# Performance work log

Hardware: AMD Instinct MI355X
Metric: run time of the kernel (lower is better)

## Reference

```python
import jax, jax.numpy as jnp
import numpy as np

DIM = 2048
SEQ = 8192
KSZ = 3  # L_cache


def setup_inputs() -> dict:
    key = jax.random.key(0)
    ks = jax.random.split(key, 6)
    s = 1.0 / np.sqrt(DIM)
    return {
        "x": jax.random.normal(ks[0], (1, SEQ, DIM), dtype=jnp.float32),
        "B_w": jax.random.normal(ks[1], (DIM, DIM), dtype=jnp.float32) * s,
        "C_w": jax.random.normal(ks[2], (DIM, DIM), dtype=jnp.float32) * s,
        "x_w": jax.random.normal(ks[3], (DIM, DIM), dtype=jnp.float32) * s,
        "out_w": jax.random.normal(ks[4], (DIM, DIM), dtype=jnp.float32) * s,
        "conv_w": jax.random.normal(ks[5], (DIM, 1, KSZ), dtype=jnp.float32) * (1.0 / np.sqrt(KSZ)),
        "conv_state": jnp.zeros((1, DIM, KSZ - 1), dtype=jnp.float32),
    }


def reference(x, B_w, C_w, x_w, out_w, conv_w, conv_state):
    # x: [1, S, D]; Linear(y = x @ W.T), then transpose to [1, D, S]
    B = jnp.einsum('bsd,ed->bes', x, B_w)   # [1, D, S]
    C = jnp.einsum('bsd,ed->bes', x, C_w)   # [1, D, S]
    xp = jnp.einsum('bsd,ed->bes', x, x_w)  # [1, D, S]

    Bx = B * xp                                          # gated input [1, D, S]
    Bxp = jnp.concatenate([conv_state, Bx], axis=-1)     # [1, D, S + K - 1]

    # depthwise causal conv1d, kernel size K, groups = D
    conv_out = jax.lax.conv_general_dilated(
        Bxp, conv_w,
        window_strides=(1,), padding='VALID',
        dimension_numbers=('NCH', 'OIH', 'NCH'),
        feature_group_count=DIM,
    )  # [1, D, S]

    y = C * conv_out                              # output gate [1, D, S]
    y = jnp.swapaxes(y, -1, -2)                   # [1, S, D]
    return jnp.einsum('bsd,ed->bse', y, out_w)    # out_proj [1, S, D]
```

## Files before the change

### kernel.cpp

```cpp
#include <hip/hip_runtime.h>
#include <hip/hip_bf16.h>
#include <cstdint>
#include <cstddef>

#define D_DIM 2048
#define S_SEQ 8192

typedef __attribute__((ext_vector_type(8))) short bf16x8;
typedef __attribute__((ext_vector_type(4))) float f32x4;

__device__ inline unsigned short f2b(float f) {
    __hip_bfloat16 h = __float2bfloat16(f);
    return __builtin_bit_cast(unsigned short, h);
}
__device__ inline float b2f(unsigned short u) {
    return __bfloat162float(__builtin_bit_cast(__hip_bfloat16, u));
}

__global__ __launch_bounds__(256)
void cast_f32_to_bf16(const float* __restrict__ in, unsigned short* __restrict__ out, int n4) {
    int stride = gridDim.x * blockDim.x;
    for (int i = blockIdx.x * blockDim.x + threadIdx.x; i < n4; i += stride) {
        float4 v = reinterpret_cast<const float4*>(in)[i];
        ushort4 o;
        o.x = f2b(v.x); o.y = f2b(v.y); o.z = f2b(v.z); o.w = f2b(v.w);
        reinterpret_cast<ushort4*>(out)[i] = o;
    }
}

template<int MODE>
__global__ __launch_bounds__(256, 2)
void gemm_bt(const unsigned short* __restrict__ A,
             const unsigned short* __restrict__ W,
             void* out,
             const unsigned short* prev,
             int M, int N, int K)
{
    __shared__ unsigned short As[128][40];
    __shared__ unsigned short Ws[128][40];

    const int t    = threadIdx.x;
    const int lane = t & 63;
    const int wave = t >> 6;
    const int wr   = wave >> 1;
    const int wc   = wave & 1;

    const int row0 = blockIdx.x * 128;
    const int col0 = blockIdx.y * 128;

    f32x4 acc[4][4] = {};

    const int rl = lane & 15;
    const int kg = (lane >> 4) * 8;

    for (int k0 = 0; k0 < K; k0 += 32) {
        #pragma unroll
        for (int r = 0; r < 2; ++r) {
            int idx = r * 256 + t;
            int row = idx >> 2;
            int col = (idx & 3) << 3;
            *reinterpret_cast<bf16x8*>(&As[row][col]) =
                *reinterpret_cast<const bf16x8*>(&A[(size_t)(row0 + row) * K + k0 + col]);
            *reinterpret_cast<bf16x8*>(&Ws[row][col]) =
                *reinterpret_cast<const bf16x8*>(&W[(size_t)(col0 + row) * K + k0 + col]);
        }
        __syncthreads();

        bf16x8 a[4], b[4];
        #pragma unroll
        for (int m = 0; m < 4; ++m)
            a[m] = *reinterpret_cast<const bf16x8*>(&As[wr * 64 + m * 16 + rl][kg]);
        #pragma unroll
        for (int n = 0; n < 4; ++n)
            b[n] = *reinterpret_cast<const bf16x8*>(&Ws[wc * 64 + n * 16 + rl][kg]);

        #pragma unroll
        for (int m = 0; m < 4; ++m)
            #pragma unroll
            for (int n = 0; n < 4; ++n)
                acc[m][n] = __builtin_amdgcn_mfma_f32_16x16x32_bf16(a[m], b[n], acc[m][n], 0, 0, 0);

        __syncthreads();
    }

    const int cr = (lane >> 4) * 4;
    const int cc = lane & 15;
    #pragma unroll
    for (int m = 0; m < 4; ++m) {
        #pragma unroll
        for (int n = 0; n < 4; ++n) {
            int gr = row0 + wr * 64 + m * 16 + cr;
            int gc = col0 + wc * 64 + n * 16 + cc;
            #pragma unroll
            for (int r = 0; r < 4; ++r) {
                size_t off = (size_t)(gr + r) * N + gc;
                float v = acc[m][n][r];
                if (MODE == 0) {
                    ((unsigned short*)out)[off] = f2b(v);
                } else if (MODE == 1) {
                    ((unsigned short*)out)[off] = f2b(v * b2f(prev[off]));
                } else {
                    ((float*)out)[off] = v;
                }
            }
        }
    }
}

__global__ __launch_bounds__(256)
void conv_gate(const unsigned short* __restrict__ bx,
               const unsigned short* __restrict__ cb,
               const float* __restrict__ conv_w,
               const float* __restrict__ state,
               unsigned short* __restrict__ y)
{
    int s  = blockIdx.x;
    int d0 = threadIdx.x << 3;

    bf16x8 vc = *reinterpret_cast<const bf16x8*>(&bx[(size_t)s * D_DIM + d0]);
    bf16x8 vC = *reinterpret_cast<const bf16x8*>(&cb[(size_t)s * D_DIM + d0]);

    float x1[8], x2[8];
    if (s >= 2) {
        bf16x8 v1 = *reinterpret_cast<const bf16x8*>(&bx[(size_t)(s - 1) * D_DIM + d0]);
        bf16x8 v2 = *reinterpret_cast<const bf16x8*>(&bx[(size_t)(s - 2) * D_DIM + d0]);
        #pragma unroll
        for (int j = 0; j < 8; ++j) { x1[j] = b2f((unsigned short)v1[j]); x2[j] = b2f((unsigned short)v2[j]); }
    } else if (s == 1) {
        bf16x8 v1 = *reinterpret_cast<const bf16x8*>(&bx[(size_t)0 * D_DIM + d0]);
        #pragma unroll
        for (int j = 0; j < 8; ++j) { x1[j] = b2f((unsigned short)v1[j]); x2[j] = state[(d0 + j) * 2 + 1]; }
    } else {
        #pragma unroll
        for (int j = 0; j < 8; ++j) { x1[j] = state[(d0 + j) * 2 + 1]; x2[j] = state[(d0 + j) * 2 + 0]; }
    }

    bf16x8 o;
    #pragma unroll
    for (int j = 0; j < 8; ++j) {
        int d = d0 + j;
        float cur = b2f((unsigned short)vc[j]);
        float co  = conv_w[d * 3 + 0] * x2[j]
                  + conv_w[d * 3 + 1] * x1[j]
                  + conv_w[d * 3 + 2] * cur;
        o[j] = (short)f2b(b2f((unsigned short)vC[j]) * co);
    }
    *reinterpret_cast<bf16x8*>(&y[(size_t)s * D_DIM + d0]) = o;
}

extern "C" void kernel_launch(void* const* d_in, const int* in_sizes, int n_in,
                              void* d_out, int out_size, void* d_ws, size_t ws_size,
                              hipStream_t stream) {
    const float* x         = (const float*)d_in[0];
    const float* B_w       = (const float*)d_in[1];
    const float* C_w       = (const float*)d_in[2];
    const float* x_w       = (const float*)d_in[3];
    const float* out_w     = (const float*)d_in[4];
    const float* conv_w    = (const float*)d_in[5];
    const float* conv_state= (const float*)d_in[6];

    const size_t SD = (size_t)S_SEQ * D_DIM;
    const size_t DD = (size_t)D_DIM * D_DIM;

    unsigned short* ws   = (unsigned short*)d_ws;
    unsigned short* xb   = ws;
    unsigned short* bwb  = xb + SD;
    unsigned short* cwb  = bwb + DD;
    unsigned short* xwb  = cwb + DD;
    unsigned short* owb  = xwb + DD;
    unsigned short* bx   = owb + DD;
    unsigned short* cbuf = bx + SD;
    unsigned short* yb   = xb;

    cast_f32_to_bf16<<<2048, 256, 0, stream>>>(x,     xb,  (int)(SD / 4));
    cast_f32_to_bf16<<<1024, 256, 0, stream>>>(B_w,   bwb, (int)(DD / 4));
    cast_f32_to_bf16<<<1024, 256, 0, stream>>>(C_w,   cwb, (int)(DD / 4));
    cast_f32_to_bf16<<<1024, 256, 0, stream>>>(x_w,   xwb, (int)(DD / 4));
    cast_f32_to_bf16<<<1024, 256, 0, stream>>>(out_w, owb, (int)(DD / 4));

    dim3 grid(S_SEQ / 128, D_DIM / 128);
    gemm_bt<0><<<grid, 256, 0, stream>>>(xb, bwb, bx,   nullptr, S_SEQ, D_DIM, D_DIM);
    gemm_bt<1><<<grid, 256, 0, stream>>>(xb, xwb, bx,   bx,      S_SEQ, D_DIM, D_DIM);
    gemm_bt<0><<<grid, 256, 0, stream>>>(xb, cwb, cbuf, nullptr, S_SEQ, D_DIM, D_DIM);

    conv_gate<<<S_SEQ, 256, 0, stream>>>(bx, cbuf, conv_w, conv_state, yb);

    gemm_bt<2><<<grid, 256, 0, stream>>>(yb, owb, d_out, nullptr, S_SEQ, D_DIM, D_DIM);
}
```

Before: 553.2 us.

## Use direct global-to-LDS loads in GEMM and move B*xp gating into conv kernel

The GEMM tile loads now use global_load_lds to write straight into unpadded LDS tiles instead of staging through registers, and the occupancy hint in launch bounds is dropped. The B*xp product is no longer fused into the second GEMM epilogue; xp is written to the output buffer as scratch, and the conv kernel computes the gate itself. The conv kernel now processes 8 sequence steps per block, carrying the previous two inputs in registers and loading conv weights once. Removing the padding may cause LDS bank conflicts on the MFMA operand reads, and the conv kernel now reads an extra tensor.

```diff
diff --git a/kernel.cpp b/kernel.cpp
--- a/kernel.cpp
+++ b/kernel.cpp
@@ -9,12 +9,19 @@
 typedef __attribute__((ext_vector_type(8))) short bf16x8;
 typedef __attribute__((ext_vector_type(4))) float f32x4;
 
+#define GAS __attribute__((address_space(1)))
+#define LAS __attribute__((address_space(3)))
+
 __device__ inline unsigned short f2b(float f) {
     __hip_bfloat16 h = __float2bfloat16(f);
     return __builtin_bit_cast(unsigned short, h);
 }
 __device__ inline float b2f(unsigned short u) {
     return __bfloat162float(__builtin_bit_cast(__hip_bfloat16, u));
+}
+
+__device__ inline void gload_lds16(const unsigned short* g, unsigned short* l) {
+    __builtin_amdgcn_global_load_lds((const GAS void*)g, (LAS void*)l, 16, 0, 0);
 }
 
 __global__ __launch_bounds__(256)
@@ -29,15 +36,14 @@
 }
 
 template<int MODE>
-__global__ __launch_bounds__(256, 2)
+__global__ __launch_bounds__(256)
 void gemm_bt(const unsigned short* __restrict__ A,
              const unsigned short* __restrict__ W,
-             void* out,
-             const unsigned short* prev,
+             void* __restrict__ out,
              int M, int N, int K)
 {
-    __shared__ unsigned short As[128][40];
-    __shared__ unsigned short Ws[128][40];
+    __shared__ unsigned short As[128 * 32];
+    __shared__ unsigned short Ws[128 * 32];
 
     const int t    = threadIdx.x;
     const int lane = t & 63;
@@ -48,6 +54,9 @@
     const int row0 = blockIdx.x * 128;
     const int col0 = blockIdx.y * 128;
 
+    const int srow = lane >> 2;
+    const int scol = (lane & 3) << 3;
+
     f32x4 acc[4][4] = {};
 
     const int rl = lane & 15;
@@ -55,24 +64,22 @@
 
     for (int k0 = 0; k0 < K; k0 += 32) {
         #pragma unroll
-        for (int r = 0; r < 2; ++r) {
-            int idx = r * 256 + t;
-            int row = idx >> 2;
-            int col = (idx & 3) << 3;
-            *reinterpret_cast<bf16x8*>(&As[row][col]) =
-                *reinterpret_cast<const bf16x8*>(&A[(size_t)(row0 + row) * K + k0 + col]);
-            *reinterpret_cast<bf16x8*>(&Ws[row][col]) =
-                *reinterpret_cast<const bf16x8*>(&W[(size_t)(col0 + row) * K + k0 + col]);
+        for (int j = 0; j < 2; ++j) {
+            const int rbase = wave * 32 + j * 16;
+            gload_lds16(&A[(size_t)(row0 + rbase + srow) * K + k0 + scol],
+                        &As[rbase * 32]);
+            gload_lds16(&W[(size_t)(col0 + rbase + srow) * K + k0 + scol],
+                        &Ws[rbase * 32]);
         }
         __syncthreads();
 
         bf16x8 a[4], b[4];
         #pragma unroll
         for (int m = 0; m < 4; ++m)
-            a[m] = *reinterpret_cast<const bf16x8*>(&As[wr * 64 + m * 16 + rl][kg]);
+            a[m] = *reinterpret_cast<const bf16x8*>(&As[(wr * 64 + m * 16 + rl) * 32 + kg]);
         #pragma unroll
         for (int n = 0; n < 4; ++n)
-            b[n] = *reinterpret_cast<const bf16x8*>(&Ws[wc * 64 + n * 16 + rl][kg]);
+            b[n] = *reinterpret_cast<const bf16x8*>(&Ws[(wc * 64 + n * 16 + rl) * 32 + kg]);
 
         #pragma unroll
         for (int m = 0; m < 4; ++m)
@@ -97,8 +104,6 @@
                 float v = acc[m][n][r];
                 if (MODE == 0) {
                     ((unsigned short*)out)[off] = f2b(v);
-                } else if (MODE == 1) {
-                    ((unsigned short*)out)[off] = f2b(v * b2f(prev[off]));
                 } else {
                     ((float*)out)[off] = v;
                 }
@@ -107,57 +112,73 @@
     }
 }
 
+#define CONV_CHUNK 8
 __global__ __launch_bounds__(256)
-void conv_gate(const unsigned short* __restrict__ bx,
-               const unsigned short* __restrict__ cb,
+void conv_gate(const unsigned short* __restrict__ Bp,
+               const unsigned short* __restrict__ XPp,
+               const unsigned short* __restrict__ Cp,
                const float* __restrict__ conv_w,
                const float* __restrict__ state,
                unsigned short* __restrict__ y)
 {
-    int s  = blockIdx.x;
-    int d0 = threadIdx.x << 3;
-
-    bf16x8 vc = *reinterpret_cast<const bf16x8*>(&bx[(size_t)s * D_DIM + d0]);
-    bf16x8 vC = *reinterpret_cast<const bf16x8*>(&cb[(size_t)s * D_DIM + d0]);
-
-    float x1[8], x2[8];
-    if (s >= 2) {
-        bf16x8 v1 = *reinterpret_cast<const bf16x8*>(&bx[(size_t)(s - 1) * D_DIM + d0]);
-        bf16x8 v2 = *reinterpret_cast<const bf16x8*>(&bx[(size_t)(s - 2) * D_DIM + d0]);
-        #pragma unroll
-        for (int j = 0; j < 8; ++j) { x1[j] = b2f((unsigned short)v1[j]); x2[j] = b2f((unsigned short)v2[j]); }
-    } else if (s == 1) {
-        bf16x8 v1 = *reinterpret_cast<const bf16x8*>(&bx[(size_t)0 * D_DIM + d0]);
-        #pragma unroll
-        for (int j = 0; j < 8; ++j) { x1[j] = b2f((unsigned short)v1[j]); x2[j] = state[(d0 + j) * 2 + 1]; }
-    } else {
-        #pragma unroll
-        for (int j = 0; j < 8; ++j) { x1[j] = state[(d0 + j) * 2 + 1]; x2[j] = state[(d0 + j) * 2 + 0]; }
-    }
-
-    bf16x8 o;
+    const int s0 = blockIdx.x * CONV_CHUNK;
+    const int d0 = threadIdx.x << 3;
+
+    float w0[8], w1[8], w2[8];
     #pragma unroll
     for (int j = 0; j < 8; ++j) {
         int d = d0 + j;
-        float cur = b2f((unsigned short)vc[j]);
-        float co  = conv_w[d * 3 + 0] * x2[j]
-                  + conv_w[d * 3 + 1] * x1[j]
-                  + conv_w[d * 3 + 2] * cur;
-        o[j] = (short)f2b(b2f((unsigned short)vC[j]) * co);
-    }
-    *reinterpret_cast<bf16x8*>(&y[(size_t)s * D_DIM + d0]) = o;
+        w0[j] = conv_w[d * 3 + 0];
+        w1[j] = conv_w[d * 3 + 1];
+        w2[j] = conv_w[d * 3 + 2];
+    }
+
+    float p1[8], p2[8];
+    if (s0 >= 2) {
+        bf16x8 b2v  = *reinterpret_cast<const bf16x8*>(&Bp [(size_t)(s0 - 2) * D_DIM + d0]);
+        bf16x8 x2v  = *reinterpret_cast<const bf16x8*>(&XPp[(size_t)(s0 - 2) * D_DIM + d0]);
+        bf16x8 b1v  = *reinterpret_cast<const bf16x8*>(&Bp [(size_t)(s0 - 1) * D_DIM + d0]);
+        bf16x8 x1v  = *reinterpret_cast<const bf16x8*>(&XPp[(size_t)(s0 - 1) * D_DIM + d0]);
+        #pragma unroll
+        for (int j = 0; j < 8; ++j) {
+            p2[j] = b2f((unsigned short)b2v[j]) * b2f((unsigned short)x2v[j]);
+            p1[j] = b2f((unsigned short)b1v[j]) * b2f((unsigned short)x1v[j]);
+        }
+    } else {
+        #pragma unroll
+        for (int j = 0; j < 8; ++j) {
+            p2[j] = state[(d0 + j) * 2 + 0];
+            p1[j] = state[(d0 + j) * 2 + 1];
+        }
+    }
+
+    for (int s = s0; s < s0 + CONV_CHUNK; ++s) {
+        bf16x8 bv = *reinterpret_cast<const bf16x8*>(&Bp [(size_t)s * D_DIM + d0]);
+        bf16x8 xv = *reinterpret_cast<const bf16x8*>(&XPp[(size_t)s * D_DIM + d0]);
+        bf16x8 cv = *reinterpret_cast<const bf16x8*>(&Cp [(size_t)s * D_DIM + d0]);
+        bf16x8 o;
+        #pragma unroll
+        for (int j = 0; j < 8; ++j) {
+            float cur = b2f((unsigned short)bv[j]) * b2f((unsigned short)xv[j]);
+            float co  = w0[j] * p2[j] + w1[j] * p1[j] + w2[j] * cur;
+            o[j] = (short)f2b(b2f((unsigned short)cv[j]) * co);
+            p2[j] = p1[j];
+            p1[j] = cur;
+        }
+        *reinterpret_cast<bf16x8*>(&y[(size_t)s * D_DIM + d0]) = o;
+    }
 }
 
 extern "C" void kernel_launch(void* const* d_in, const int* in_sizes, int n_in,
                               void* d_out, int out_size, void* d_ws, size_t ws_size,
                               hipStream_t stream) {
-    const float* x         = (const float*)d_in[0];
-    const float* B_w       = (const float*)d_in[1];
-    const float* C_w       = (const float*)d_in[2];
-    const float* x_w       = (const float*)d_in[3];
-    const float* out_w     = (const float*)d_in[4];
-    const float* conv_w    = (const float*)d_in[5];
-    const float* conv_state= (const float*)d_in[6];
+    const float* x          = (const float*)d_in[0];
+    const float* B_w        = (const float*)d_in[1];
+    const float* C_w        = (const float*)d_in[2];
+    const float* x_w        = (const float*)d_in[3];
+    const float* out_w      = (const float*)d_in[4];
+    const float* conv_w     = (const float*)d_in[5];
+    const float* conv_state = (const float*)d_in[6];
 
     const size_t SD = (size_t)S_SEQ * D_DIM;
     const size_t DD = (size_t)D_DIM * D_DIM;
@@ -170,6 +191,7 @@
     unsigned short* owb  = xwb + DD;
     unsigned short* bx   = owb + DD;
     unsigned short* cbuf = bx + SD;
+    unsigned short* xpb  = (unsigned short*)d_out;
     unsigned short* yb   = xb;
 
     cast_f32_to_bf16<<<2048, 256, 0, stream>>>(x,     xb,  (int)(SD / 4));
@@ -179,11 +201,11 @@
     cast_f32_to_bf16<<<1024, 256, 0, stream>>>(out_w, owb, (int)(DD / 4));
 
     dim3 grid(S_SEQ / 128, D_DIM / 128);
-    gemm_bt<0><<<grid, 256, 0, stream>>>(xb, bwb, bx,   nullptr, S_SEQ, D_DIM, D_DIM);
-    gemm_bt<1><<<grid, 256, 0, stream>>>(xb, xwb, bx,   bx,      S_SEQ, D_DIM, D_DIM);
-    gemm_bt<0><<<grid, 256, 0, stream>>>(xb, cwb, cbuf, nullptr, S_SEQ, D_DIM, D_DIM);
-
-    conv_gate<<<S_SEQ, 256, 0, stream>>>(bx, cbuf, conv_w, conv_state, yb);
-
-    gemm_bt<2><<<grid, 256, 0, stream>>>(yb, owb, d_out, nullptr, S_SEQ, D_DIM, D_DIM);
-}
+    gemm_bt<0><<<grid, 256, 0, stream>>>(xb, bwb, bx,   S_SEQ, D_DIM, D_DIM);
+    gemm_bt<0><<<grid, 256, 0, stream>>>(xb, xwb, xpb,  S_SEQ, D_DIM, D_DIM);
+    gemm_bt<0><<<grid, 256, 0, stream>>>(xb, cwb, cbuf, S_SEQ, D_DIM, D_DIM);
+
+    conv_gate<<<S_SEQ / CONV_CHUNK, 256, 0, stream>>>(bx, xpb, cbuf, conv_w, conv_state, yb);
+
+    gemm_bt<2><<<grid, 256, 0, stream>>>(yb, owb, d_out, S_SEQ, D_DIM, D_DIM);
+}
```

After: 609.7 us. 10.2% more time.
